# Performance work log

Measured on AMD Instinct MI355X. Metric: run time of the kernel, lower is better.

## Reference

```python
import jax, jax.numpy as jnp
import numpy as np

N = 4096      # nodes
D = 256       # input_dim
OUT = 256     # output_dim
K = 4         # num_kernels
TOPK = 16
CHEB_T = 2
ROW_TEMP = 1.0
EPS = 1e-9


def setup_inputs() -> dict:
    key = jax.random.key(0)
    ks = jax.random.split(key, 6)
    X = jax.random.normal(ks[0], (N, D), dtype=jnp.float32)
    L_k = jax.random.normal(ks[1], (K, D, D), dtype=jnp.float32) * 0.02
    alpha = jnp.ones((K,), dtype=jnp.float32)
    theta = jax.random.normal(ks[2], (CHEB_T + 1, D), dtype=jnp.float32) * 0.02
    rho_raw = jnp.zeros((), dtype=jnp.float32)
    proj_w = jax.random.normal(ks[3], (OUT, D), dtype=jnp.float32) / np.float32(np.sqrt(D))
    proj_b = jnp.zeros((OUT,), dtype=jnp.float32)
    v0 = jax.random.normal(ks[4], (N, 1), dtype=jnp.float32)  # power-iteration init
    return dict(X=X, L_k=L_k, alpha=alpha, theta=theta, rho_raw=rho_raw,
                proj_w=proj_w, proj_b=proj_b, v0=v0)


def reference(X, L_k, alpha, theta, rho_raw, proj_w, proj_b, v0):
    n, d = X.shape
    k = L_k.shape[0]
    # 1) kernel stack: A_k = X L_k X^T / sqrt(D), row softmax  -> (K,N,N)
    A = jnp.einsum('nd,kde,me->knm', X, L_k, X) / jnp.sqrt(jnp.float32(d))
    H_stack = jax.nn.softmax(A / max(ROW_TEMP, 1e-6), axis=-1)
    w = jax.nn.softmax(alpha)[:, None, None]
    H_fused = (H_stack * w).sum(0)                               # (N,N)
    # 2) soft incidence via per-row top-k + renormalize, scattered into B (N, K*N)
    vals, idx = jax.lax.top_k(H_stack, TOPK)                     # (K,N,TOPK)
    vals = vals / (vals.sum(-1, keepdims=True) + EPS)
    E = k * n
    cols = jnp.arange(k)[:, None, None] * n + jnp.arange(n)[None, :, None]
    cols = jnp.broadcast_to(cols, idx.shape)
    B = jnp.zeros((n, E), X.dtype).at[idx.reshape(-1), cols.reshape(-1)].set(vals.reshape(-1))
    W = jnp.ones((E,), X.dtype)
    # 3) hypergraph Laplacian L = I - Dv^{-1/2} B W De^{-1} B^T Dv^{-1/2}
    De = B.sum(0) + EPS
    Dv = (B * W[None, :]).sum(1) + EPS
    Dv_is = 1.0 / jnp.sqrt(Dv)
    S = (B * (W / De)[None, :]) @ B.T                            # (N,N)
    S_norm = Dv_is[:, None] * S * Dv_is[None, :]
    L = jnp.eye(n, dtype=X.dtype) - S_norm
    # 4) lambda_max via power iteration on detached L (constant, as in torch)
    Ld = jax.lax.stop_gradient(L)
    v = v0 / (jnp.linalg.norm(v0) + EPS)
    for _ in range(5):
        v = Ld @ v
        v = v / (jnp.linalg.norm(v) + EPS)
    lam = jnp.maximum((v.T @ (Ld @ v)).squeeze(), jnp.float32(1e-3))
    lam = jax.lax.stop_gradient(lam)
    # Chebyshev filter
    L_tilde = (2.0 / lam) * L - jnp.eye(n, dtype=X.dtype)
    out = X * theta[0][None, :]
    T0 = X
    T1 = L_tilde @ X
    out = out + T1 * theta[1][None, :]
    for t in range(2, CHEB_T + 1):
        T2 = 2.0 * (L_tilde @ T1) - T0
        out = out + T2 * theta[t][None, :]
        T0, T1 = T1, T2
    Z_spec = jax.nn.elu(out)
    # 5) residual blend with kernel diffusion
    Z_kern = H_fused @ X
    rho = jax.nn.sigmoid(rho_raw)
    Z_mix = rho * Z_spec + (1.0 - rho) * Z_kern
    # 6) final projection
    return Z_mix @ proj_w.T + proj_b[None, :]
```

## Files before the change

kernel.cpp:

```cpp
#include <hip/hip_runtime.h>
#include <math.h>

#define N_ 4096
#define D_ 256
#define K_ 4
#define TK_ 16
#define E_ (K_ * N_)
#define NENT_ (E_ * TK_)

typedef unsigned short u16;
typedef unsigned int u32;
typedef __attribute__((ext_vector_type(8))) short bf16x8;
typedef __attribute__((ext_vector_type(4))) float f32x4;

__device__ __forceinline__ u16 bf16_rne(float x) {
  u32 u = __float_as_uint(x);
  u32 r = u + 0x7FFFu + ((u >> 16) & 1u);
  return (u16)(r >> 16);
}


__global__ void scalars_kernel(const float* __restrict__ alpha,
                               const float* __restrict__ rho_raw,
                               float* __restrict__ scal) {
  if (threadIdx.x == 0) {
    float m = alpha[0];
    for (int k = 1; k < K_; ++k) m = fmaxf(m, alpha[k]);
    float e[K_]; float s = 0.f;
    for (int k = 0; k < K_; ++k) { e[k] = expf(alpha[k] - m); s += e[k]; }
    for (int k = 0; k < K_; ++k) scal[k] = e[k] / s;
    scal[4] = 1.0f / (1.0f + expf(-rho_raw[0]));
  }
}

__global__ void dvis_kernel(const float* __restrict__ DvAcc, float* __restrict__ Dvis) {
  int i = blockIdx.x * 256 + threadIdx.x;
  Dvis[i] = 1.0f / sqrtf(DvAcc[i] + 1e-9f);
}

__global__ void make_tkvd(const float* __restrict__ tkv, const int* __restrict__ tki,
                          const float* __restrict__ Dvis, float* __restrict__ tkvd) {
  int i = blockIdx.x * 256 + threadIdx.x;
  tkvd[i] = tkv[i] * Dvis[tki[i]];
}

__global__ void cvt_split4(const float* __restrict__ in, u16* __restrict__ hi,
                           u16* __restrict__ lo) {
  int i = (blockIdx.x * 256 + threadIdx.x) * 4;
  float4 v = *(const float4*)(in + i);
  u16 h0 = bf16_rne(v.x), h1 = bf16_rne(v.y), h2 = bf16_rne(v.z), h3 = bf16_rne(v.w);
  float f0 = __uint_as_float((u32)h0 << 16), f1 = __uint_as_float((u32)h1 << 16);
  float f2 = __uint_as_float((u32)h2 << 16), f3 = __uint_as_float((u32)h3 << 16);
  u16 l0 = bf16_rne(v.x - f0), l1 = bf16_rne(v.y - f1);
  u16 l2 = bf16_rne(v.z - f2), l3 = bf16_rne(v.w - f3);
  *(uint2*)(hi + i) = make_uint2((u32)h0 | ((u32)h1 << 16), (u32)h2 | ((u32)h3 << 16));
  *(uint2*)(lo + i) = make_uint2((u32)l0 | ((u32)l1 << 16), (u32)l2 | ((u32)l3 << 16));
}

__global__ __launch_bounds__(256) void transpose_split(const float* __restrict__ X,
                                                       u16* __restrict__ ht,
                                                       u16* __restrict__ lt) {
  __shared__ float tile[32][33];
  const int tx = threadIdx.x & 31, ty = threadIdx.x >> 5;
  const int d0 = blockIdx.x * 32, n0 = blockIdx.y * 32;
#pragma unroll
  for (int q = 0; q < 4; ++q)
    tile[ty + q * 8][tx] = X[(size_t)(n0 + ty + q * 8) * D_ + d0 + tx];
  __syncthreads();
#pragma unroll
  for (int q = 0; q < 4; ++q) {
    int dd = ty + q * 8;
    float v = tile[tx][dd];
    u16 h = bf16_rne(v);
    float hf = __uint_as_float((u32)h << 16);
    u16 l = bf16_rne(v - hf);
    ht[(size_t)(d0 + dd) * N_ + n0 + tx] = h;
    lt[(size_t)(d0 + dd) * N_ + n0 + tx] = l;
  }
}

__global__ __launch_bounds__(256) void gemm_nn64_split(const float* __restrict__ A,
                                                       const float* __restrict__ B,
                                                       u16* __restrict__ Ch,
                                                       u16* __restrict__ Cl,
                                                       int Kdim, int lda, int ldb, int ldc) {
  __shared__ float As[16][68];
  __shared__ float Bs[16][68];
  const int tid = threadIdx.x;
  const int bm = blockIdx.x * 64, bn = blockIdx.y * 64;
  const int lrA = tid >> 2, lcA = (tid & 3) * 4;
  const int rrB = tid >> 4, ccB = (tid & 15) * 4;
  const int tx = tid & 15, ty = tid >> 4;
  const float* Ap = A + (size_t)(bm + lrA) * lda + lcA;
  const float* Bp = B + (size_t)rrB * ldb + bn + ccB;
  float acc[4][4] = {};
  for (int k0 = 0; k0 < Kdim; k0 += 16) {
    float4 av = *(const float4*)(Ap + k0);
    float4 bv = *(const float4*)(Bp + (size_t)k0 * ldb);
    __syncthreads();
    As[lcA + 0][lrA] = av.x; As[lcA + 1][lrA] = av.y;
    As[lcA + 2][lrA] = av.z; As[lcA + 3][lrA] = av.w;
    *(float4*)&Bs[rrB][ccB] = bv;
    __syncthreads();
#pragma unroll
    for (int kk = 0; kk < 16; ++kk) {
      float a[4], b[4];
      *(float4*)a = *(const float4*)&As[kk][ty * 4];
      *(float4*)b = *(const float4*)&Bs[kk][tx * 4];
#pragma unroll
      for (int i = 0; i < 4; ++i)
#pragma unroll
        for (int j = 0; j < 4; ++j) acc[i][j] += a[i] * b[j];
    }
  }
#pragma unroll
  for (int i = 0; i < 4; ++i) {
    int row = bm + ty * 4 + i;
    u16 h[4], lo[4];
#pragma unroll
    for (int j = 0; j < 4; ++j) {
      h[j] = bf16_rne(acc[i][j]);
      lo[j] = bf16_rne(acc[i][j] - __uint_as_float((u32)h[j] << 16));
    }
    size_t base = (size_t)row * ldc + bn + tx * 4;
    *(uint2*)(Ch + base) = make_uint2((u32)h[0] | ((u32)h[1] << 16), (u32)h[2] | ((u32)h[3] << 16));
    *(uint2*)(Cl + base) = make_uint2((u32)lo[0] | ((u32)lo[1] << 16), (u32)lo[2] | ((u32)lo[3] << 16));
  }
}

__global__ __launch_bounds__(256) void gemm_nt64_bias(const float* __restrict__ A,
                                                      const float* __restrict__ B,
                                                      const float* __restrict__ bias,
                                                      float* __restrict__ C,
                                                      int Kdim, int lda, int ldb, int ldc) {
  __shared__ float As[16][68];
  __shared__ float Bs[16][68];
  const int tid = threadIdx.x;
  const int bm = blockIdx.x * 64, bn = blockIdx.y * 64;
  const int lr = tid >> 2, lc = (tid & 3) * 4;
  const int tx = tid & 15, ty = tid >> 4;
  const float* Ap = A + (size_t)(bm + lr) * lda + lc;
  const float* Bp = B + (size_t)(bn + lr) * ldb + lc;
  float acc[4][4] = {};
  for (int k0 = 0; k0 < Kdim; k0 += 16) {
    float4 av = *(const float4*)(Ap + k0);
    float4 bv = *(const float4*)(Bp + k0);
    __syncthreads();
    As[lc + 0][lr] = av.x; As[lc + 1][lr] = av.y; As[lc + 2][lr] = av.z; As[lc + 3][lr] = av.w;
    Bs[lc + 0][lr] = bv.x; Bs[lc + 1][lr] = bv.y; Bs[lc + 2][lr] = bv.z; Bs[lc + 3][lr] = bv.w;
    __syncthreads();
#pragma unroll
    for (int kk = 0; kk < 16; ++kk) {
      float a[4], b[4];
      *(float4*)a = *(const float4*)&As[kk][ty * 4];
      *(float4*)b = *(const float4*)&Bs[kk][tx * 4];
#pragma unroll
      for (int i = 0; i < 4; ++i)
#pragma unroll
        for (int j = 0; j < 4; ++j) acc[i][j] += a[i] * b[j];
    }
  }
#pragma unroll
  for (int i = 0; i < 4; ++i) {
    int row = bm + ty * 4 + i;
    float4 o;
    o.x = acc[i][0] + bias[bn + tx * 4 + 0];
    o.y = acc[i][1] + bias[bn + tx * 4 + 1];
    o.z = acc[i][2] + bias[bn + tx * 4 + 2];
    o.w = acc[i][3] + bias[bn + tx * 4 + 3];
    *(float4*)(C + (size_t)row * ldc + bn + tx * 4) = o;
  }
}


__global__ __launch_bounds__(256) void scores_mfma(const u16* __restrict__ Ahg,
                                                   const u16* __restrict__ Alg,
                                                   const u16* __restrict__ Bhg,
                                                   const u16* __restrict__ Blg,
                                                   float* __restrict__ C, float scale) {
  __shared__ char smem[65536];
  const int tid = threadIdx.x;
  const int bm = blockIdx.x * 128, bn = blockIdx.y * 128;
  const int w = tid >> 6, l = tid & 63;
  const int wr = (w >> 1) * 64, wc = (w & 1) * 64;
  const int srow = tid >> 3, scol = (tid & 7) * 8;
  const int lb = l & 15, lke = (l >> 4) * 8;
  const u16* bh0 = Bhg + (size_t)(bn + wc + 0  + lb) * D_ + lke;
  const u16* bh1 = Bhg + (size_t)(bn + wc + 16 + lb) * D_ + lke;
  const u16* bh2 = Bhg + (size_t)(bn + wc + 32 + lb) * D_ + lke;
  const u16* bh3 = Bhg + (size_t)(bn + wc + 48 + lb) * D_ + lke;
  const size_t dlo = (size_t)(Blg - Bhg);
  const int aoff[4] = {
    (srow + 0)  * 128 + ((scol * 2) ^ (((srow + 0)  & 7) << 4)),
    (srow + 32) * 128 + ((scol * 2) ^ (((srow + 32) & 7) << 4)),
    (srow + 64) * 128 + ((scol * 2) ^ (((srow + 64) & 7) << 4)),
    (srow + 96) * 128 + ((scol * 2) ^ (((srow + 96) & 7) << 4)) };
  f32x4 acc[4][4];
#pragma unroll
  for (int i = 0; i < 4; ++i)
#pragma unroll
    for (int j = 0; j < 4; ++j) { acc[i][j][0] = 0.f; acc[i][j][1] = 0.f; acc[i][j][2] = 0.f; acc[i][j][3] = 0.f; }

  uint4 ah[4], al[4];
#pragma unroll
  for (int ii = 0; ii < 4; ++ii) {
    int r = srow + ii * 32;
    ah[ii] = *(const uint4*)(Ahg + (size_t)(bm + r) * D_ + scol);
    al[ii] = *(const uint4*)(Alg + (size_t)(bm + r) * D_ + scol);
  }
  {
    char* bAh = smem; char* bAl = smem + 16384;
#pragma unroll
    for (int ii = 0; ii < 4; ++ii) {
      *(uint4*)(bAh + aoff[ii]) = ah[ii];
      *(uint4*)(bAl + aoff[ii]) = al[ii];
    }
  }
  __syncthreads();

  for (int c = 0; c < 4; ++c) {
    char* bAh = smem + ((c & 1) << 15);
    char* bAl = bAh + 16384;
    const bool hn = (c < 3);
    if (hn) {
      const int kn = (c + 1) * 64;
#pragma unroll
      for (int ii = 0; ii < 4; ++ii) {
        int r = srow + ii * 32;
        ah[ii] = *(const uint4*)(Ahg + (size_t)(bm + r) * D_ + kn + scol);
        al[ii] = *(const uint4*)(Alg + (size_t)(bm + r) * D_ + kn + scol);
      }
    }
#pragma unroll
    for (int kk = 0; kk < 2; ++kk) {
      const int kb = kk * 64 + ((l >> 4) << 4);
      const int ge = c * 64 + kk * 32;
      bf16x8 fbh[4], fbl[4];
      fbh[0] = *(const bf16x8*)(bh0 + ge); fbl[0] = *(const bf16x8*)(bh0 + dlo + ge);
      fbh[1] = *(const bf16x8*)(bh1 + ge); fbl[1] = *(const bf16x8*)(bh1 + dlo + ge);
      fbh[2] = *(const bf16x8*)(bh2 + ge); fbl[2] = *(const bf16x8*)(bh2 + dlo + ge);
      fbh[3] = *(const bf16x8*)(bh3 + ge); fbl[3] = *(const bf16x8*)(bh3 + dlo + ge);
#pragma unroll
      for (int i = 0; i < 4; ++i) {
        int ra = wr + i * 16 + lb;
        int oa = ra * 128 + (kb ^ ((ra & 7) << 4));
        bf16x8 fah = *(const bf16x8*)(bAh + oa);
        bf16x8 fal = *(const bf16x8*)(bAl + oa);
#pragma unroll
        for (int j = 0; j < 4; ++j) {
          acc[i][j] = __builtin_amdgcn_mfma_f32_16x16x32_bf16(fah, fbh[j], acc[i][j], 0, 0, 0);
          acc[i][j] = __builtin_amdgcn_mfma_f32_16x16x32_bf16(fah, fbl[j], acc[i][j], 0, 0, 0);
          acc[i][j] = __builtin_amdgcn_mfma_f32_16x16x32_bf16(fal, fbh[j], acc[i][j], 0, 0, 0);
        }
      }
    }
    if (hn) {
      char* nAh = smem + (((c + 1) & 1) << 15);
      char* nAl = nAh + 16384;
#pragma unroll
      for (int ii = 0; ii < 4; ++ii) {
        *(uint4*)(nAh + aoff[ii]) = ah[ii];
        *(uint4*)(nAl + aoff[ii]) = al[ii];
      }
    }
    __syncthreads();
  }
  float* Cs = (float*)smem;
  const int cr = (l >> 4) * 4, cc = l & 15;
#pragma unroll
  for (int p = 0; p < 2; ++p) {
    __syncthreads();
    if ((w >> 1) == p) {
#pragma unroll
      for (int i = 0; i < 4; ++i)
#pragma unroll
        for (int r = 0; r < 4; ++r) {
          int rl = i * 16 + cr + r;
          int sw = ((rl >> 2) & 3) << 4;
#pragma unroll
          for (int j = 0; j < 4; ++j) {
            int cl = wc + j * 16 + cc;
            Cs[rl * 128 + (cl ^ sw)] = acc[i][j][r] * scale;
          }
        }
    }
    __syncthreads();
#pragma unroll
    for (int ii = 0; ii < 8; ++ii) {
      int rl = ii * 8 + (tid >> 5);
      int c4 = (tid & 31) * 4;
      float4 v = *(float4*)&Cs[rl * 128 + (c4 ^ (((rl >> 2) & 3) << 4))];
      *(float4*)(C + (size_t)(bm + p * 64 + rl) * N_ + bn + c4) = v;
    }
  }
}

__global__ __launch_bounds__(256) void zkern_mfma(const u16* __restrict__ Hb,
                                                  const float* __restrict__ rowZ,
                                                  const u16* __restrict__ BhT,
                                                  const u16* __restrict__ BlT,
                                                  float* __restrict__ Zpart,
                                                  const float* __restrict__ scal,
                                                  int kidx, int kchunk, int accum) {
  __shared__ char smem[32768];
  const int tid = threadIdx.x;
  const int bm = blockIdx.x * 128, bn = blockIdx.y * 128;
  const int kz = blockIdx.z;
  const int w = tid >> 6, l = tid & 63;
  const int wr = (w >> 1) * 64, wc = (w & 1) * 64;
  const int hrow = tid >> 4, hcol = (tid & 15) * 4;
  const int lb = l & 15, lke = (l >> 4) * 8;
  const u16* bh0 = BhT + (size_t)(bn + wc + 0  + lb) * N_ + lke;
  const u16* bh1 = BhT + (size_t)(bn + wc + 16 + lb) * N_ + lke;
  const u16* bh2 = BhT + (size_t)(bn + wc + 32 + lb) * N_ + lke;
  const u16* bh3 = BhT + (size_t)(bn + wc + 48 + lb) * N_ + lke;
  const size_t dlo = (size_t)(BlT - BhT);
  int aoff[8];
#pragma unroll
  for (int ii = 0; ii < 8; ++ii) {
    int r = hrow + ii * 16;
    aoff[ii] = r * 128 + ((hcol * 2) ^ ((r & 7) << 4));
  }
  f32x4 acc[4][4];
#pragma unroll
  for (int i = 0; i < 4; ++i)
#pragma unroll
    for (int j = 0; j < 4; ++j) { acc[i][j][0] = 0.f; acc[i][j][1] = 0.f; acc[i][j][2] = 0.f; acc[i][j][3] = 0.f; }

  const int nchunk = kchunk >> 6;
  const int kbase = kz * kchunk;

  uint2 hv[8];
#pragma unroll
  for (int ii = 0; ii < 8; ++ii)
    hv[ii] = *(const uint2*)(Hb + (size_t)(bm + hrow + ii * 16) * N_ + kbase + hcol);
  {
    char* bAh = smem;
#pragma unroll
    for (int ii = 0; ii < 8; ++ii) *(uint2*)(bAh + aoff[ii]) = hv[ii];
  }
  __syncthreads();

  for (int c = 0; c < nchunk; ++c) {
    char* bAh = smem + ((c & 1) << 14);
    const bool hn = (c + 1 < nchunk);
    if (hn) {
      const int kn = kbase + (c + 1) * 64;
#pragma unroll
      for (int ii = 0; ii < 8; ++ii)
        hv[ii] = *(const uint2*)(Hb + (size_t)(bm + hrow + ii * 16) * N_ + kn + hcol);
    }
#pragma unroll
    for (int kk = 0; kk < 2; ++kk) {
      const int kb = kk * 64 + ((l >> 4) << 4);
      const int ge = kbase + c * 64 + kk * 32;
      bf16x8 fbh[4], fbl[4];
      fbh[0] = *(const bf16x8*)(bh0 + ge); fbl[0] = *(const bf16x8*)(bh0 + dlo + ge);
      fbh[1] = *(const bf16x8*)(bh1 + ge); fbl[1] = *(const bf16x8*)(bh1 + dlo + ge);
      fbh[2] = *(const bf16x8*)(bh2 + ge); fbl[2] = *(const bf16x8*)(bh2 + dlo + ge);
      fbh[3] = *(const bf16x8*)(bh3 + ge); fbl[3] = *(const bf16x8*)(bh3 + dlo + ge);
#pragma unroll
      for (int i = 0; i < 4; ++i) {
        int ra = wr + i * 16 + lb;
        int oa = ra * 128 + (kb ^ ((ra & 7) << 4));
        bf16x8 fah = *(const bf16x8*)(bAh + oa);
#pragma unroll
        for (int j = 0; j < 4; ++j) {
          acc[i][j] = __builtin_amdgcn_mfma_f32_16x16x32_bf16(fah, fbh[j], acc[i][j], 0, 0, 0);
          acc[i][j] = __builtin_amdgcn_mfma_f32_16x16x32_bf16(fah, fbl[j], acc[i][j], 0, 0, 0);
        }
      }
    }
    if (hn) {
      char* nAh = smem + (((c + 1) & 1) << 14);
#pragma unroll
      for (int ii = 0; ii < 8; ++ii) *(uint2*)(nAh + aoff[ii]) = hv[ii];
    }
    __syncthreads();
  }
  const float wk = scal[kidx];
  float* Zp = Zpart + (size_t)kz * N_ * D_;
  float* Cs = (float*)smem;
  const int cr = (l >> 4) * 4, cc = l & 15;
#pragma unroll
  for (int p = 0; p < 2; ++p) {
    __syncthreads();
    if ((w >> 1) == p) {
#pragma unroll
      for (int i = 0; i < 4; ++i)
#pragma unroll
        for (int r = 0; r < 4; ++r) {
          int rl = i * 16 + cr + r;
          int sw = ((rl >> 2) & 3) << 4;
#pragma unroll
          for (int j = 0; j < 4; ++j) {
            int cl = wc + j * 16 + cc;
            Cs[rl * 128 + (cl ^ sw)] = acc[i][j][r];
          }
        }
    }
    __syncthreads();
#pragma unroll
    for (int ii = 0; ii < 8; ++ii) {
      int rl = ii * 8 + (tid >> 5);
      int c4 = (tid & 31) * 4;
      int row = bm + p * 64 + rl;
      float sc = wk / rowZ[row];
      float4 v = *(float4*)&Cs[rl * 128 + (c4 ^ (((rl >> 2) & 3) << 4))];
      float* zb = Zp + (size_t)row * D_ + bn + c4;
      if (accum) {
        float4 z = *(float4*)zb;
        z.x += sc * v.x; z.y += sc * v.y; z.z += sc * v.z; z.w += sc * v.w;
        *(float4*)zb = z;
      } else {
        float4 z;
        z.x = sc * v.x; z.y = sc * v.y; z.z = sc * v.z; z.w = sc * v.w;
        *(float4*)zb = z;
      }
    }
  }
}

__global__ __launch_bounds__(256) void rowstats_topk(const float* __restrict__ S,
                                                     float* __restrict__ rowmax,
                                                     float* __restrict__ rowZ,
                                                     u16* __restrict__ Hb,
                                                     float* __restrict__ tkv,
                                                     int* __restrict__ tki) {
  const int row = blockIdx.x, tid = threadIdx.x;
  const int wid = tid >> 6, lane = tid & 63;
  __shared__ int hist[1024];
  __shared__ int P[256];
  __shared__ float cval[256];
  __shared__ int cgi[256];
  __shared__ int ccnt;
  __shared__ int binlo_s;
  __shared__ float rv[4];
  __shared__ float stk[TK_];
  __shared__ int itk[TK_];
  __shared__ float tv16[TK_];
  __shared__ float mzs[3];

  hist[tid] = 0; hist[tid + 256] = 0; hist[tid + 512] = 0; hist[tid + 768] = 0;
  if (tid == 0) ccnt = 0;

  const float4* Sp = (const float4*)(S + (size_t)row * N_);
  float r[16];
  float lmax = -3.4e38f;
#pragma unroll
  for (int it = 0; it < 4; ++it) {
    float4 v = Sp[tid + it * 256];
    r[it * 4 + 0] = v.x; r[it * 4 + 1] = v.y; r[it * 4 + 2] = v.z; r[it * 4 + 3] = v.w;
    lmax = fmaxf(lmax, fmaxf(fmaxf(v.x, v.y), fmaxf(v.z, v.w)));
  }
#pragma unroll
  for (int off = 32; off; off >>= 1) lmax = fmaxf(lmax, __shfl_xor(lmax, off));
  if (lane == 0) rv[wid] = lmax;
  __syncthreads();
  if (tid == 0) mzs[0] = fmaxf(fmaxf(rv[0], rv[1]), fmaxf(rv[2], rv[3]));
  __syncthreads();
  const float M = mzs[0];
  float eh[16];
  float ls = 0.f;
#pragma unroll
  for (int j = 0; j < 16; ++j) { eh[j] = expf(r[j] - M); ls += eh[j]; }
#pragma unroll
  for (int off = 32; off; off >>= 1) ls += __shfl_xor(ls, off);
  if (lane == 0) rv[wid] = ls;
  __syncthreads();
  if (tid == 0) {
    float z = rv[0] + rv[1] + rv[2] + rv[3];
    mzs[1] = z; rowmax[row] = M; rowZ[row] = z;
  }
  u16* Hrow = Hb + (size_t)row * N_;
#pragma unroll
  for (int it = 0; it < 4; ++it) {
    u16 h0 = bf16_rne(eh[it * 4 + 0]), h1 = bf16_rne(eh[it * 4 + 1]);
    u16 h2 = bf16_rne(eh[it * 4 + 2]), h3 = bf16_rne(eh[it * 4 + 3]);
    *(uint2*)(Hrow + it * 1024 + tid * 4) =
        make_uint2((u32)h0 | ((u32)h1 << 16), (u32)h2 | ((u32)h3 << 16));
  }
  __syncthreads();
  const float Z = mzs[1];

#pragma unroll
  for (int j = 0; j < 16; ++j) {
    u32 u = __float_as_uint(r[j]);
    u32 key = (u >> 31) ? ~u : (u | 0x80000000u);
    atomicAdd(&hist[key >> 22], 1);
  }
  __syncthreads();
  const int b0 = tid * 4;
  const int h0 = hist[b0], h1 = hist[b0 + 1], h2 = hist[b0 + 2], h3 = hist[b0 + 3];
  P[tid] = h0 + h1 + h2 + h3;
  __syncthreads();
  for (int o = 1; o < 256; o <<= 1) {
    int v = P[tid] + ((tid + o < 256) ? P[tid + o] : 0);
    __syncthreads();
    P[tid] = v;
    __syncthreads();
  }
  {
    int above = (tid < 255) ? P[tid + 1] : 0;
    int s3 = above + h3, s2 = s3 + h2, s1 = s2 + h1, s0 = s1 + h0;
    if (s3 >= TK_ && above < TK_) binlo_s = b0 + 3;
    else if (s2 >= TK_ && s3 < TK_) binlo_s = b0 + 2;
    else if (s1 >= TK_ && s2 < TK_) binlo_s = b0 + 1;
    else if (s0 >= TK_ && s1 < TK_) binlo_s = b0;
  }
  __syncthreads();
  const u32 kmin = (u32)binlo_s << 22;
#pragma unroll
  for (int j = 0; j < 16; ++j) {
    u32 u = __float_as_uint(r[j]);
    u32 key = (u >> 31) ? ~u : (u | 0x80000000u);
    if (key >= kmin) {
      int p = atomicAdd(&ccnt, 1);
      if (p < 256) {
        cval[p] = r[j];
        cgi[p] = 4 * tid + ((j >> 2) << 10) + (j & 3);
      }
    }
  }
  __syncthreads();
  const int nc = min(ccnt, 256);
  for (int t = 0; t < TK_; ++t) {
    if (tid < 64) {
      float bv = -3.4e38f; int bg = 0x7fffffff, bp = -1;
      for (int p = tid; p < nc; p += 64) {
        float v = cval[p]; int g = cgi[p];
        if (v > bv || (v == bv && g < bg)) { bv = v; bg = g; bp = p; }
      }
#pragma unroll
      for (int off = 32; off; off >>= 1) {
        float ov = __shfl_xor(bv, off);
        int og = __shfl_xor(bg, off);
        int op = __shfl_xor(bp, off);
        if (ov > bv || (ov == bv && og < bg)) { bv = ov; bg = og; bp = op; }
      }
      if (tid == 0) { stk[t] = bv; itk[t] = bg; cval[bp] = -3.4e38f; }
    }
    __syncthreads();
  }
  if (tid < TK_) tv16[tid] = expf(stk[tid] - M) / Z;
  __syncthreads();
  if (tid == 0) { float s = 0.f; for (int q = 0; q < TK_; ++q) s += tv16[q]; mzs[2] = s + 1e-9f; }
  __syncthreads();
  if (tid < TK_) {
    tkv[(size_t)row * TK_ + tid] = tv16[tid] / mzs[2];
    tki[(size_t)row * TK_ + tid] = itk[tid];
  }
}

__global__ void edge_scan(const float* __restrict__ tkv, const int* __restrict__ tki,
                          float* __restrict__ DvAcc, int* __restrict__ cnt,
                          float* __restrict__ invDe) {
  int e = blockIdx.x * 256 + threadIdx.x;
  float s = 0.f;
#pragma unroll
  for (int q = 0; q < TK_; ++q) s += tkv[(size_t)e * TK_ + q];
  invDe[e] = 1.0f / (s + 1e-9f);
#pragma unroll
  for (int q = 0; q < TK_; ++q) {
    int m = tki[(size_t)e * TK_ + q];
    atomicAdd(&DvAcc[m], tkv[(size_t)e * TK_ + q]);
    atomicAdd(&cnt[m], 1);
  }
}

__global__ __launch_bounds__(1024) void scan_offsets(const int* __restrict__ cnt,
                                                     int* __restrict__ off,
                                                     int* __restrict__ cur) {
  __shared__ int part[1024];
  const int t = threadIdx.x;
  const int b = t * 4;
  int c0 = cnt[b], c1 = cnt[b + 1], c2 = cnt[b + 2], c3 = cnt[b + 3];
  part[t] = c0 + c1 + c2 + c3;
  __syncthreads();
  for (int o = 1; o < 1024; o <<= 1) {
    int v = part[t] + ((t >= o) ? part[t - o] : 0);
    __syncthreads();
    part[t] = v;
    __syncthreads();
  }
  int ex = (t == 0) ? 0 : part[t - 1];
  off[b] = ex; off[b + 1] = ex + c0; off[b + 2] = ex + c0 + c1; off[b + 3] = ex + c0 + c1 + c2;
  cur[b] = off[b]; cur[b + 1] = off[b + 1]; cur[b + 2] = off[b + 2]; cur[b + 3] = off[b + 3];
  if (t == 1023) off[N_] = part[1023];
}

__global__ void edge_fill(const float* __restrict__ tkv, const int* __restrict__ tki,
                          int* __restrict__ cur, int* __restrict__ ince,
                          float* __restrict__ incv) {
  int e = blockIdx.x * 256 + threadIdx.x;
#pragma unroll
  for (int q = 0; q < TK_; ++q) {
    int m = tki[(size_t)e * TK_ + q];
    int pos = atomicAdd(&cur[m], 1);
    ince[pos] = e;
    incv[pos] = tkv[(size_t)e * TK_ + q];
  }
}

__global__ void pi_ye(const float* __restrict__ v, const float* __restrict__ tkvd,
                      const int* __restrict__ tki, const float* __restrict__ invDe,
                      float* __restrict__ ye) {
  int e = blockIdx.x * 256 + threadIdx.x;
  const float* tv = tkvd + (size_t)e * TK_;
  const int* ti = tki + (size_t)e * TK_;
  float a = 0.f;
#pragma unroll
  for (int q = 0; q < TK_; ++q) a += tv[q] * v[ti[q]];
  ye[e] = a * invDe[e];
}

__global__ void pi_step(const float* __restrict__ v, const float* __restrict__ ye,
                        const int* __restrict__ off, const int* __restrict__ ince,
                        const float* __restrict__ incv, const float* __restrict__ Dvis,
                        float* __restrict__ vn) {
  int m = blockIdx.x * 256 + threadIdx.x;
  float z = 0.f;
  int j0 = off[m], j1 = off[m + 1];
  for (int j = j0; j < j1; ++j) z += incv[j] * ye[ince[j]];
  vn[m] = v[m] - Dvis[m] * z;
}

__global__ __launch_bounds__(256) void pi_final(const float* __restrict__ v,
                                                const float* __restrict__ ye,
                                                const int* __restrict__ off,
                                                const int* __restrict__ ince,
                                                const float* __restrict__ incv,
                                                const float* __restrict__ Dvis,
                                                float* __restrict__ partial) {
  __shared__ float r1[256], r2[256];
  int m = blockIdx.x * 256 + threadIdx.x;
  float z = 0.f;
  int j0 = off[m], j1 = off[m + 1];
  for (int j = j0; j < j1; ++j) z += incv[j] * ye[ince[j]];
  float wv = v[m] - Dvis[m] * z;
  r1[threadIdx.x] = v[m] * wv;
  r2[threadIdx.x] = v[m] * v[m];
  __syncthreads();
  for (int s = 128; s; s >>= 1) {
    if (threadIdx.x < s) { r1[threadIdx.x] += r1[threadIdx.x + s]; r2[threadIdx.x] += r2[threadIdx.x + s]; }
    __syncthreads();
  }
  if (threadIdx.x == 0) { partial[blockIdx.x * 2] = r1[0]; partial[blockIdx.x * 2 + 1] = r2[0]; }
}

__global__ void pi_lam(const float* __restrict__ partial, float* __restrict__ scal) {
  if (threadIdx.x == 0) {
    float s1 = 0.f, s2 = 0.f;
    for (int b = 0; b < N_ / 256; ++b) { s1 += partial[2 * b]; s2 += partial[2 * b + 1]; }
    scal[5] = fmaxf(s1 / s2, 1e-3f);
  }
}

__global__ __launch_bounds__(256) void ye_mat(const float* __restrict__ M,
                                              const float* __restrict__ tkvd,
                                              const int* __restrict__ tki,
                                              const float* __restrict__ invDe,
                                              float* __restrict__ Ye) {
  const int w = threadIdx.x >> 6, l = threadIdx.x & 63;
  const int e = blockIdx.x * 4 + w;
  const float* tv = tkvd + (size_t)e * TK_;
  const int* ti = tki + (size_t)e * TK_;
  float4 a = make_float4(0.f, 0.f, 0.f, 0.f);
#pragma unroll
  for (int q = 0; q < TK_; ++q) {
    float v = tv[q];
    const float4 x = *(const float4*)(M + (size_t)ti[q] * D_ + l * 4);
    a.x += v * x.x; a.y += v * x.y; a.z += v * x.z; a.w += v * x.w;
  }
  const float s = invDe[e];
  float4 o; o.x = a.x * s; o.y = a.y * s; o.z = a.z * s; o.w = a.w * s;
  *(float4*)(Ye + (size_t)e * D_ + l * 4) = o;
}

__global__ __launch_bounds__(256) void bgather_combine(const float* __restrict__ Ye,
                                                       const int* __restrict__ off,
                                                       const int* __restrict__ ince,
                                                       const float* __restrict__ incv,
                                                       const float* __restrict__ Dvis,
                                                       const float* __restrict__ Mx,
                                                       const float* __restrict__ G,
                                                       const float* __restrict__ scal,
                                                       float* __restrict__ out, int mode) {
  const int w = threadIdx.x >> 6, l = threadIdx.x & 63;
  const int m = blockIdx.x * 4 + w;
  const int j0 = off[m], j1 = off[m + 1];
  float4 z = make_float4(0.f, 0.f, 0.f, 0.f);
  int j = j0;
  for (; j + 2 <= j1; j += 2) {
    float v0 = incv[j];     int e0 = ince[j];
    float v1 = incv[j + 1]; int e1 = ince[j + 1];
    float4 y0 = *(const float4*)(Ye + (size_t)e0 * D_ + l * 4);
    float4 y1 = *(const float4*)(Ye + (size_t)e1 * D_ + l * 4);
    z.x += v0 * y0.x + v1 * y1.x;
    z.y += v0 * y0.y + v1 * y1.y;
    z.z += v0 * y0.z + v1 * y1.z;
    z.w += v0 * y0.w + v1 * y1.w;
  }
  if (j < j1) {
    float v0 = incv[j]; int e0 = ince[j];
    float4 y0 = *(const float4*)(Ye + (size_t)e0 * D_ + l * 4);
    z.x += v0 * y0.x; z.y += v0 * y0.y; z.z += v0 * y0.z; z.w += v0 * y0.w;
  }
  const float lam = scal[5];
  const float c = 2.0f / lam;
  const float dv = Dvis[m];
  const size_t idx = (size_t)m * D_ + l * 4;
  float4 mx = *(const float4*)(Mx + idx);
  float4 o;
  if (mode == 1) {
    o.x = (c - 1.0f) * mx.x - c * dv * z.x;
    o.y = (c - 1.0f) * mx.y - c * dv * z.y;
    o.z = (c - 1.0f) * mx.z - c * dv * z.z;
    o.w = (c - 1.0f) * mx.w - c * dv * z.w;
  } else {
    float4 g = *(const float4*)(G + idx);
    o.x = (2.0f * c - 2.0f) * mx.x - 2.0f * c * dv * z.x - g.x;
    o.y = (2.0f * c - 2.0f) * mx.y - 2.0f * c * dv * z.y - g.y;
    o.z = (2.0f * c - 2.0f) * mx.z - 2.0f * c * dv * z.z - g.z;
    o.w = (2.0f * c - 2.0f) * mx.w - 2.0f * c * dv * z.w - g.w;
  }
  *(float4*)(out + idx) = o;
}

__global__ void mix_kernel(const float* __restrict__ X, const float* __restrict__ T1,
                           const float* __restrict__ T2, const float* __restrict__ theta,
                           const float* __restrict__ Zpart, int splitk,
                           const float* __restrict__ scal, float* __restrict__ Zmix) {
  const int i = blockIdx.x * 256 + threadIdx.x;
  const int d = i & (D_ - 1);
  float cheb = X[i] * theta[d] + T1[i] * theta[D_ + d] + T2[i] * theta[2 * D_ + d];
  float zs = cheb > 0.f ? cheb : expm1f(cheb);
  float zk = 0.f;
  for (int s = 0; s < splitk; ++s) zk += Zpart[(size_t)s * N_ * D_ + i];
  const float rho = scal[4];
  Zmix[i] = rho * zs + (1.0f - rho) * zk;
}


extern "C" void kernel_launch(void* const* d_in, const int* in_sizes, int n_in,
                              void* d_out, int out_size, void* d_ws, size_t ws_size,
                              hipStream_t stream) {
  const float* X       = (const float*)d_in[0];
  const float* L_k     = (const float*)d_in[1];
  const float* alpha   = (const float*)d_in[2];
  const float* theta   = (const float*)d_in[3];
  const float* rho_raw = (const float*)d_in[4];
  const float* proj_w  = (const float*)d_in[5];
  const float* proj_b  = (const float*)d_in[6];
  const float* v0      = (const float*)d_in[7];
  float* out = (float*)d_out;

  char* w = (char*)d_ws;
  size_t o = 0;
  auto alloc = [&](size_t bytes) -> char* {
    char* p = w + o; o += (bytes + 255) & ~(size_t)255; return p;
  };
  float* S     = (float*)alloc((size_t)N_ * N_ * 4);
  u16*   Hb    = (u16*)  alloc((size_t)N_ * N_ * 2);
  u16*   Xh    = (u16*)  alloc((size_t)N_ * D_ * 2);
  u16*   Xl    = (u16*)  alloc((size_t)N_ * D_ * 2);
  u16*   XhT   = (u16*)  alloc((size_t)D_ * N_ * 2);
  u16*   XlT   = (u16*)  alloc((size_t)D_ * N_ * 2);
  u16*   XLh   = (u16*)  alloc((size_t)N_ * D_ * 2);
  u16*   XLl   = (u16*)  alloc((size_t)N_ * D_ * 2);
  float* rowmax= (float*)alloc(N_ * 4);
  float* rowZ  = (float*)alloc(N_ * 4);
  float* tkv   = (float*)alloc((size_t)NENT_ * 4);
  int*   tki   = (int*)  alloc((size_t)NENT_ * 4);
  float* tkvd  = (float*)alloc((size_t)NENT_ * 4);
  float* invDe = (float*)alloc(E_ * 4);
  float* DvAcc = (float*)alloc(N_ * 4);
  float* Dvis  = (float*)alloc(N_ * 4);
  int*   cnt   = (int*)  alloc(N_ * 4);
  int*   off   = (int*)  alloc((N_ + 1) * 4);
  int*   cur   = (int*)  alloc(N_ * 4);
  int*   ince  = (int*)  alloc((size_t)NENT_ * 4);
  float* incv  = (float*)alloc((size_t)NENT_ * 4);
  float* va    = (float*)alloc(N_ * 4);
  float* vbuf  = (float*)alloc(N_ * 4);
  float* yev   = (float*)alloc(E_ * 4);
  float* part  = (float*)alloc((N_ / 256) * 2 * 4);
  float* scal  = (float*)alloc(256);
  int SPLITK = 8;
  while (SPLITK > 1 && o + (size_t)SPLITK * N_ * D_ * 4 > ws_size) SPLITK >>= 1;
  float* Zpart = (float*)alloc((size_t)SPLITK * N_ * D_ * 4);
  const int kchunk = N_ / SPLITK;
  float* Ye   = S + (size_t)N_ * D_;
  float* T1   = Ye + (size_t)E_ * D_;
  float* T2   = T1 + (size_t)N_ * D_;
  float* Zmix = T2 + (size_t)N_ * D_;

  scalars_kernel<<<1, 64, 0, stream>>>(alpha, rho_raw, scal);
  hipMemsetAsync(DvAcc, 0, N_ * 4, stream);
  hipMemsetAsync(cnt, 0, N_ * 4, stream);

  cvt_split4<<<(N_ * D_ / 4) / 256, 256, 0, stream>>>(X, Xh, Xl);
  transpose_split<<<dim3(D_ / 32, N_ / 32), 256, 0, stream>>>(X, XhT, XlT);

  for (int k = 0; k < K_; ++k) {
    gemm_nn64_split<<<dim3(N_ / 64, D_ / 64), 256, 0, stream>>>(
        X, L_k + (size_t)k * D_ * D_, XLh, XLl, D_, D_, D_, D_);
    scores_mfma<<<dim3(N_ / 128, N_ / 128), 256, 0, stream>>>(
        XLh, XLl, Xh, Xl, S, 1.0f / 16.0f);
    rowstats_topk<<<N_, 256, 0, stream>>>(
        S, rowmax, rowZ, Hb, tkv + (size_t)k * N_ * TK_, tki + (size_t)k * N_ * TK_);
    zkern_mfma<<<dim3(N_ / 128, D_ / 128, SPLITK), 256, 0, stream>>>(
        Hb, rowZ, XhT, XlT, Zpart, scal, k, kchunk, (k > 0) ? 1 : 0);
  }

  edge_scan<<<E_ / 256, 256, 0, stream>>>(tkv, tki, DvAcc, cnt, invDe);
  dvis_kernel<<<N_ / 256, 256, 0, stream>>>(DvAcc, Dvis);
  make_tkvd<<<NENT_ / 256, 256, 0, stream>>>(tkv, tki, Dvis, tkvd);
  scan_offsets<<<1, 1024, 0, stream>>>(cnt, off, cur);
  edge_fill<<<E_ / 256, 256, 0, stream>>>(tkv, tki, cur, ince, incv);

  const float* vc = v0;
  float* vn = va;
  for (int it = 0; it < 5; ++it) {
    pi_ye<<<E_ / 256, 256, 0, stream>>>(vc, tkvd, tki, invDe, yev);
    pi_step<<<N_ / 256, 256, 0, stream>>>(vc, yev, off, ince, incv, Dvis, vn);
    vc = vn;
    vn = (vc == va) ? vbuf : va;
  }
  pi_ye<<<E_ / 256, 256, 0, stream>>>(vc, tkvd, tki, invDe, yev);
  pi_final<<<N_ / 256, 256, 0, stream>>>(vc, yev, off, ince, incv, Dvis, part);
  pi_lam<<<1, 64, 0, stream>>>(part, scal);

  ye_mat<<<E_ / 4, 256, 0, stream>>>(X, tkvd, tki, invDe, Ye);
  bgather_combine<<<N_ / 4, 256, 0, stream>>>(Ye, off, ince, incv, Dvis, X, X, scal, T1, 1);
  ye_mat<<<E_ / 4, 256, 0, stream>>>(T1, tkvd, tki, invDe, Ye);
  bgather_combine<<<N_ / 4, 256, 0, stream>>>(Ye, off, ince, incv, Dvis, T1, X, scal, T2, 2);

  mix_kernel<<<N_ * D_ / 256, 256, 0, stream>>>(X, T1, T2, theta, Zpart, SPLITK, scal, Zmix);

  gemm_nt64_bias<<<dim3(N_ / 64, D_ / 64), 256, 0, stream>>>(
      Zmix, proj_w, proj_b, out, D_, D_, D_, D_);
}
```

Measured before the change: 1.191 ms.

## Use MFMA for X·L_k and fuse power iteration into one cooperative kernel

Replaces the fp32 SIMT GEMM computing X·L_k with a bf16 split-precision MFMA kernel. L_k is pre-transposed and split once into high and low bf16 parts. Separately, the twelve small power-iteration launches are merged into one cooperative kernel that uses grid-wide syncs between steps, cutting launch overhead. The cooperative launch needs all 64 blocks to be co-resident, and the three-term bf16 split adds a small precision change.

```diff
diff --git a/kernel.cpp b/kernel.cpp
--- a/kernel.cpp
+++ b/kernel.cpp
@@ -1,4 +1,5 @@
 #include <hip/hip_runtime.h>
+#include <hip/hip_cooperative_groups.h>
 #include <math.h>
 
 #define N_ 4096
@@ -79,52 +80,28 @@
   }
 }
 
-__global__ __launch_bounds__(256) void gemm_nn64_split(const float* __restrict__ A,
-                                                       const float* __restrict__ B,
-                                                       u16* __restrict__ Ch,
-                                                       u16* __restrict__ Cl,
-                                                       int Kdim, int lda, int ldb, int ldc) {
-  __shared__ float As[16][68];
-  __shared__ float Bs[16][68];
-  const int tid = threadIdx.x;
-  const int bm = blockIdx.x * 64, bn = blockIdx.y * 64;
-  const int lrA = tid >> 2, lcA = (tid & 3) * 4;
-  const int rrB = tid >> 4, ccB = (tid & 15) * 4;
-  const int tx = tid & 15, ty = tid >> 4;
-  const float* Ap = A + (size_t)(bm + lrA) * lda + lcA;
-  const float* Bp = B + (size_t)rrB * ldb + bn + ccB;
-  float acc[4][4] = {};
-  for (int k0 = 0; k0 < Kdim; k0 += 16) {
-    float4 av = *(const float4*)(Ap + k0);
-    float4 bv = *(const float4*)(Bp + (size_t)k0 * ldb);
-    __syncthreads();
-    As[lcA + 0][lrA] = av.x; As[lcA + 1][lrA] = av.y;
-    As[lcA + 2][lrA] = av.z; As[lcA + 3][lrA] = av.w;
-    *(float4*)&Bs[rrB][ccB] = bv;
-    __syncthreads();
-#pragma unroll
-    for (int kk = 0; kk < 16; ++kk) {
-      float a[4], b[4];
-      *(float4*)a = *(const float4*)&As[kk][ty * 4];
-      *(float4*)b = *(const float4*)&Bs[kk][tx * 4];
-#pragma unroll
-      for (int i = 0; i < 4; ++i)
-#pragma unroll
-        for (int j = 0; j < 4; ++j) acc[i][j] += a[i] * b[j];
-    }
-  }
-#pragma unroll
-  for (int i = 0; i < 4; ++i) {
-    int row = bm + ty * 4 + i;
-    u16 h[4], lo[4];
-#pragma unroll
-    for (int j = 0; j < 4; ++j) {
-      h[j] = bf16_rne(acc[i][j]);
-      lo[j] = bf16_rne(acc[i][j] - __uint_as_float((u32)h[j] << 16));
-    }
-    size_t base = (size_t)row * ldc + bn + tx * 4;
-    *(uint2*)(Ch + base) = make_uint2((u32)h[0] | ((u32)h[1] << 16), (u32)h[2] | ((u32)h[3] << 16));
-    *(uint2*)(Cl + base) = make_uint2((u32)lo[0] | ((u32)lo[1] << 16), (u32)lo[2] | ((u32)lo[3] << 16));
+__global__ __launch_bounds__(256) void transpose_split_L(const float* __restrict__ L,
+                                                         u16* __restrict__ lth,
+                                                         u16* __restrict__ ltl) {
+  __shared__ float tile[32][33];
+  const int tx = threadIdx.x & 31, ty = threadIdx.x >> 5;
+  const int n0 = blockIdx.x * 32, k0 = blockIdx.y * 32, kk = blockIdx.z;
+  const float* Lk = L + (size_t)kk * D_ * D_;
+#pragma unroll
+  for (int q = 0; q < 4; ++q)
+    tile[ty + q * 8][tx] = Lk[(size_t)(k0 + ty + q * 8) * D_ + n0 + tx];
+  __syncthreads();
+  u16* ho = lth + (size_t)kk * D_ * D_;
+  u16* lo = ltl + (size_t)kk * D_ * D_;
+#pragma unroll
+  for (int q = 0; q < 4; ++q) {
+    int nn = ty + q * 8;
+    float v = tile[tx][nn];
+    u16 h = bf16_rne(v);
+    float hf = __uint_as_float((u32)h << 16);
+    u16 l = bf16_rne(v - hf);
+    ho[(size_t)(n0 + nn) * D_ + k0 + tx] = h;
+    lo[(size_t)(n0 + nn) * D_ + k0 + tx] = l;
   }
 }
 
@@ -172,6 +149,138 @@
   }
 }
 
+
+__global__ __launch_bounds__(256) void xl_mfma(const u16* __restrict__ Ahg,
+                                               const u16* __restrict__ Alg,
+                                               const u16* __restrict__ Bhg,
+                                               const u16* __restrict__ Blg,
+                                               u16* __restrict__ Ch,
+                                               u16* __restrict__ Cl) {
+  __shared__ char smem[65536];
+  const int tid = threadIdx.x;
+  const int bm = blockIdx.x * 128, bn = blockIdx.y * 128;
+  const int w = tid >> 6, l = tid & 63;
+  const int wr = (w >> 1) * 64, wc = (w & 1) * 64;
+  const int srow = tid >> 3, scol = (tid & 7) * 8;
+  const int lb = l & 15, lke = (l >> 4) * 8;
+  const u16* bh0 = Bhg + (size_t)(bn + wc + 0  + lb) * D_ + lke;
+  const u16* bh1 = Bhg + (size_t)(bn + wc + 16 + lb) * D_ + lke;
+  const u16* bh2 = Bhg + (size_t)(bn + wc + 32 + lb) * D_ + lke;
+  const u16* bh3 = Bhg + (size_t)(bn + wc + 48 + lb) * D_ + lke;
+  const size_t dlo = (size_t)(Blg - Bhg);
+  const int aoff[4] = {
+    (srow + 0)  * 128 + ((scol * 2) ^ (((srow + 0)  & 7) << 4)),
+    (srow + 32) * 128 + ((scol * 2) ^ (((srow + 32) & 7) << 4)),
+    (srow + 64) * 128 + ((scol * 2) ^ (((srow + 64) & 7) << 4)),
+    (srow + 96) * 128 + ((scol * 2) ^ (((srow + 96) & 7) << 4)) };
+  f32x4 acc[4][4];
+#pragma unroll
+  for (int i = 0; i < 4; ++i)
+#pragma unroll
+    for (int j = 0; j < 4; ++j) { acc[i][j][0] = 0.f; acc[i][j][1] = 0.f; acc[i][j][2] = 0.f; acc[i][j][3] = 0.f; }
+
+  uint4 ah[4], al[4];
+#pragma unroll
+  for (int ii = 0; ii < 4; ++ii) {
+    int r = srow + ii * 32;
+    ah[ii] = *(const uint4*)(Ahg + (size_t)(bm + r) * D_ + scol);
+    al[ii] = *(const uint4*)(Alg + (size_t)(bm + r) * D_ + scol);
+  }
+  {
+    char* bAh = smem; char* bAl = smem + 16384;
+#pragma unroll
+    for (int ii = 0; ii < 4; ++ii) {
+      *(uint4*)(bAh + aoff[ii]) = ah[ii];
+      *(uint4*)(bAl + aoff[ii]) = al[ii];
+    }
+  }
+  __syncthreads();
+
+  for (int c = 0; c < 4; ++c) {
+    char* bAh = smem + ((c & 1) << 15);
+    char* bAl = bAh + 16384;
+    const bool hn = (c < 3);
+    if (hn) {
+      const int kn = (c + 1) * 64;
+#pragma unroll
+      for (int ii = 0; ii < 4; ++ii) {
+        int r = srow + ii * 32;
+        ah[ii] = *(const uint4*)(Ahg + (size_t)(bm + r) * D_ + kn + scol);
+        al[ii] = *(const uint4*)(Alg + (size_t)(bm + r) * D_ + kn + scol);
+      }
+    }
+#pragma unroll
+    for (int kk = 0; kk < 2; ++kk) {
+      const int kb = kk * 64 + ((l >> 4) << 4);
+      const int ge = c * 64 + kk * 32;
+      bf16x8 fbh[4], fbl[4];
+      fbh[0] = *(const bf16x8*)(bh0 + ge); fbl[0] = *(const bf16x8*)(bh0 + dlo + ge);
+      fbh[1] = *(const bf16x8*)(bh1 + ge); fbl[1] = *(const bf16x8*)(bh1 + dlo + ge);
+      fbh[2] = *(const bf16x8*)(bh2 + ge); fbl[2] = *(const bf16x8*)(bh2 + dlo + ge);
+      fbh[3] = *(const bf16x8*)(bh3 + ge); fbl[3] = *(const bf16x8*)(bh3 + dlo + ge);
+#pragma unroll
+      for (int i = 0; i < 4; ++i) {
+        int ra = wr + i * 16 + lb;
+        int oa = ra * 128 + (kb ^ ((ra & 7) << 4));
+        bf16x8 fah = *(const bf16x8*)(bAh + oa);
+        bf16x8 fal = *(const bf16x8*)(bAl + oa);
+#pragma unroll
+        for (int j = 0; j < 4; ++j) {
+          acc[i][j] = __builtin_amdgcn_mfma_f32_16x16x32_bf16(fah, fbh[j], acc[i][j], 0, 0, 0);
+          acc[i][j] = __builtin_amdgcn_mfma_f32_16x16x32_bf16(fah, fbl[j], acc[i][j], 0, 0, 0);
+          acc[i][j] = __builtin_amdgcn_mfma_f32_16x16x32_bf16(fal, fbh[j], acc[i][j], 0, 0, 0);
+        }
+      }
+    }
+    if (hn) {
+      char* nAh = smem + (((c + 1) & 1) << 15);
+      char* nAl = nAh + 16384;
+#pragma unroll
+      for (int ii = 0; ii < 4; ++ii) {
+        *(uint4*)(nAh + aoff[ii]) = ah[ii];
+        *(uint4*)(nAl + aoff[ii]) = al[ii];
+      }
+    }
+    __syncthreads();
+  }
+  float* Cs = (float*)smem;
+  const int cr = (l >> 4) * 4, cc = l & 15;
+#pragma unroll
+  for (int p = 0; p < 2; ++p) {
+    __syncthreads();
+    if ((w >> 1) == p) {
+#pragma unroll
+      for (int i = 0; i < 4; ++i)
+#pragma unroll
+        for (int r = 0; r < 4; ++r) {
+          int rl = i * 16 + cr + r;
+          int sw = ((rl >> 2) & 3) << 4;
+#pragma unroll
+          for (int j = 0; j < 4; ++j) {
+            int cl = wc + j * 16 + cc;
+            Cs[rl * 128 + (cl ^ sw)] = acc[i][j][r];
+          }
+        }
+    }
+    __syncthreads();
+#pragma unroll
+    for (int ii = 0; ii < 8; ++ii) {
+      int rl = ii * 8 + (tid >> 5);
+      int c4 = (tid & 31) * 4;
+      float4 v = *(float4*)&Cs[rl * 128 + (c4 ^ (((rl >> 2) & 3) << 4))];
+      int row = bm + p * 64 + rl;
+      u16 h0 = bf16_rne(v.x), h1 = bf16_rne(v.y), h2 = bf16_rne(v.z), h3 = bf16_rne(v.w);
+      u16 l0 = bf16_rne(v.x - __uint_as_float((u32)h0 << 16));
+      u16 l1 = bf16_rne(v.y - __uint_as_float((u32)h1 << 16));
+      u16 l2 = bf16_rne(v.z - __uint_as_float((u32)h2 << 16));
+      u16 l3 = bf16_rne(v.w - __uint_as_float((u32)h3 << 16));
+      *(uint2*)(Ch + (size_t)row * D_ + bn + c4) =
+          make_uint2((u32)h0 | ((u32)h1 << 16), (u32)h2 | ((u32)h3 << 16));
+      *(uint2*)(Cl + (size_t)row * D_ + bn + c4) =
+          make_uint2((u32)l0 | ((u32)l1 << 16), (u32)l2 | ((u32)l3 << 16));
+    }
+  }
+}
 
 __global__ __launch_bounds__(256) void scores_mfma(const u16* __restrict__ Ahg,
                                                    const u16* __restrict__ Alg,
@@ -602,54 +711,65 @@
   }
 }
 
-__global__ void pi_ye(const float* __restrict__ v, const float* __restrict__ tkvd,
-                      const int* __restrict__ tki, const float* __restrict__ invDe,
-                      float* __restrict__ ye) {
-  int e = blockIdx.x * 256 + threadIdx.x;
-  const float* tv = tkvd + (size_t)e * TK_;
-  const int* ti = tki + (size_t)e * TK_;
-  float a = 0.f;
-#pragma unroll
-  for (int q = 0; q < TK_; ++q) a += tv[q] * v[ti[q]];
-  ye[e] = a * invDe[e];
-}
-
-__global__ void pi_step(const float* __restrict__ v, const float* __restrict__ ye,
-                        const int* __restrict__ off, const int* __restrict__ ince,
-                        const float* __restrict__ incv, const float* __restrict__ Dvis,
-                        float* __restrict__ vn) {
-  int m = blockIdx.x * 256 + threadIdx.x;
-  float z = 0.f;
-  int j0 = off[m], j1 = off[m + 1];
-  for (int j = j0; j < j1; ++j) z += incv[j] * ye[ince[j]];
-  vn[m] = v[m] - Dvis[m] * z;
-}
-
-__global__ __launch_bounds__(256) void pi_final(const float* __restrict__ v,
-                                                const float* __restrict__ ye,
-                                                const int* __restrict__ off,
-                                                const int* __restrict__ ince,
-                                                const float* __restrict__ incv,
-                                                const float* __restrict__ Dvis,
-                                                float* __restrict__ partial) {
+__global__ void pi_fused(const float* __restrict__ v0, const float* __restrict__ tkvd,
+                         const int* __restrict__ tki, const float* __restrict__ invDe,
+                         const int* __restrict__ off, const int* __restrict__ ince,
+                         const float* __restrict__ incv, const float* __restrict__ Dvis,
+                         float* __restrict__ va, float* __restrict__ vb2,
+                         float* __restrict__ ye, float* __restrict__ partial,
+                         float* __restrict__ scal) {
+  namespace cg = cooperative_groups;
+  cg::grid_group g = cg::this_grid();
+  const int gid = blockIdx.x * 256 + threadIdx.x;
+  const float* vc = v0;
+  float* vn = va;
+  for (int it = 0; it < 5; ++it) {
+    {
+      const float* tv = tkvd + (size_t)gid * TK_;
+      const int* ti = tki + (size_t)gid * TK_;
+      float a = 0.f;
+#pragma unroll
+      for (int q = 0; q < TK_; ++q) a += tv[q] * vc[ti[q]];
+      ye[gid] = a * invDe[gid];
+    }
+    g.sync();
+    if (gid < N_) {
+      float z = 0.f;
+      int j0 = off[gid], j1 = off[gid + 1];
+      for (int j = j0; j < j1; ++j) z += incv[j] * ye[ince[j]];
+      vn[gid] = vc[gid] - Dvis[gid] * z;
+    }
+    g.sync();
+    vc = vn;
+    vn = (vc == va) ? vb2 : va;
+  }
+  {
+    const float* tv = tkvd + (size_t)gid * TK_;
+    const int* ti = tki + (size_t)gid * TK_;
+    float a = 0.f;
+#pragma unroll
+    for (int q = 0; q < TK_; ++q) a += tv[q] * vc[ti[q]];
+    ye[gid] = a * invDe[gid];
+  }
+  g.sync();
   __shared__ float r1[256], r2[256];
-  int m = blockIdx.x * 256 + threadIdx.x;
-  float z = 0.f;
-  int j0 = off[m], j1 = off[m + 1];
-  for (int j = j0; j < j1; ++j) z += incv[j] * ye[ince[j]];
-  float wv = v[m] - Dvis[m] * z;
-  r1[threadIdx.x] = v[m] * wv;
-  r2[threadIdx.x] = v[m] * v[m];
-  __syncthreads();
-  for (int s = 128; s; s >>= 1) {
-    if (threadIdx.x < s) { r1[threadIdx.x] += r1[threadIdx.x + s]; r2[threadIdx.x] += r2[threadIdx.x + s]; }
-    __syncthreads();
-  }
-  if (threadIdx.x == 0) { partial[blockIdx.x * 2] = r1[0]; partial[blockIdx.x * 2 + 1] = r2[0]; }
-}
-
-__global__ void pi_lam(const float* __restrict__ partial, float* __restrict__ scal) {
-  if (threadIdx.x == 0) {
+  if (blockIdx.x < N_ / 256) {
+    int m = gid;
+    float z = 0.f;
+    int j0 = off[m], j1 = off[m + 1];
+    for (int j = j0; j < j1; ++j) z += incv[j] * ye[ince[j]];
+    float wv = vc[m] - Dvis[m] * z;
+    r1[threadIdx.x] = vc[m] * wv;
+    r2[threadIdx.x] = vc[m] * vc[m];
+    __syncthreads();
+    for (int s = 128; s; s >>= 1) {
+      if (threadIdx.x < s) { r1[threadIdx.x] += r1[threadIdx.x + s]; r2[threadIdx.x] += r2[threadIdx.x + s]; }
+      __syncthreads();
+    }
+    if (threadIdx.x == 0) { partial[blockIdx.x * 2] = r1[0]; partial[blockIdx.x * 2 + 1] = r2[0]; }
+  }
+  g.sync();
+  if (gid == 0) {
     float s1 = 0.f, s2 = 0.f;
     for (int b = 0; b < N_ / 256; ++b) { s1 += partial[2 * b]; s2 += partial[2 * b + 1]; }
     scal[5] = fmaxf(s1 / s2, 1e-3f);
@@ -718,11 +838,11 @@
     o.z = (c - 1.0f) * mx.z - c * dv * z.z;
     o.w = (c - 1.0f) * mx.w - c * dv * z.w;
   } else {
-    float4 g = *(const float4*)(G + idx);
-    o.x = (2.0f * c - 2.0f) * mx.x - 2.0f * c * dv * z.x - g.x;
-    o.y = (2.0f * c - 2.0f) * mx.y - 2.0f * c * dv * z.y - g.y;
-    o.z = (2.0f * c - 2.0f) * mx.z - 2.0f * c * dv * z.z - g.z;
-    o.w = (2.0f * c - 2.0f) * mx.w - 2.0f * c * dv * z.w - g.w;
+    float4 gg = *(const float4*)(G + idx);
+    o.x = (2.0f * c - 2.0f) * mx.x - 2.0f * c * dv * z.x - gg.x;
+    o.y = (2.0f * c - 2.0f) * mx.y - 2.0f * c * dv * z.y - gg.y;
+    o.z = (2.0f * c - 2.0f) * mx.z - 2.0f * c * dv * z.z - gg.z;
+    o.w = (2.0f * c - 2.0f) * mx.w - 2.0f * c * dv * z.w - gg.w;
   }
   *(float4*)(out + idx) = o;
 }
@@ -768,6 +888,8 @@
   u16*   XlT   = (u16*)  alloc((size_t)D_ * N_ * 2);
   u16*   XLh   = (u16*)  alloc((size_t)N_ * D_ * 2);
   u16*   XLl   = (u16*)  alloc((size_t)N_ * D_ * 2);
+  u16*   LTh   = (u16*)  alloc((size_t)K_ * D_ * D_ * 2);
+  u16*   LTl   = (u16*)  alloc((size_t)K_ * D_ * D_ * 2);
   float* rowmax= (float*)alloc(N_ * 4);
   float* rowZ  = (float*)alloc(N_ * 4);
   float* tkv   = (float*)alloc((size_t)NENT_ * 4);
@@ -801,10 +923,11 @@
 
   cvt_split4<<<(N_ * D_ / 4) / 256, 256, 0, stream>>>(X, Xh, Xl);
   transpose_split<<<dim3(D_ / 32, N_ / 32), 256, 0, stream>>>(X, XhT, XlT);
+  transpose_split_L<<<dim3(D_ / 32, D_ / 32, K_), 256, 0, stream>>>(L_k, LTh, LTl);
 
   for (int k = 0; k < K_; ++k) {
-    gemm_nn64_split<<<dim3(N_ / 64, D_ / 64), 256, 0, stream>>>(
-        X, L_k + (size_t)k * D_ * D_, XLh, XLl, D_, D_, D_, D_);
+    xl_mfma<<<dim3(N_ / 128, D_ / 128), 256, 0, stream>>>(
+        Xh, Xl, LTh + (size_t)k * D_ * D_, LTl + (size_t)k * D_ * D_, XLh, XLl);
     scores_mfma<<<dim3(N_ / 128, N_ / 128), 256, 0, stream>>>(
         XLh, XLl, Xh, Xl, S, 1.0f / 16.0f);
     rowstats_topk<<<N_, 256, 0, stream>>>(
@@ -819,17 +942,14 @@
   scan_offsets<<<1, 1024, 0, stream>>>(cnt, off, cur);
   edge_fill<<<E_ / 256, 256, 0, stream>>>(tkv, tki, cur, ince, incv);
 
-  const float* vc = v0;
-  float* vn = va;
-  for (int it = 0; it < 5; ++it) {
-    pi_ye<<<E_ / 256, 256, 0, stream>>>(vc, tkvd, tki, invDe, yev);
-    pi_step<<<N_ / 256, 256, 0, stream>>>(vc, yev, off, ince, incv, Dvis, vn);
-    vc = vn;
-    vn = (vc == va) ? vbuf : va;
-  }
-  pi_ye<<<E_ / 256, 256, 0, stream>>>(vc, tkvd, tki, invDe, yev);
-  pi_final<<<N_ / 256, 256, 0, stream>>>(vc, yev, off, ince, incv, Dvis, part);
-  pi_lam<<<1, 64, 0, stream>>>(part, scal);
+  {
+    void* pf_args[] = {(void*)&v0, (void*)&tkvd, (void*)&tki, (void*)&invDe,
+                       (void*)&off, (void*)&ince, (void*)&incv, (void*)&Dvis,
+                       (void*)&va, (void*)&vbuf, (void*)&yev, (void*)&part,
+                       (void*)&scal};
+    hipLaunchCooperativeKernel((const void*)pi_fused, dim3(E_ / 256), dim3(256),
+                               pf_args, 0, stream);
+  }
 
   ye_mat<<<E_ / 4, 256, 0, stream>>>(X, tkvd, tki, invDe, Ye);
   bgather_combine<<<N_ / 4, 256, 0, stream>>>(Ye, off, ince, incv, Dvis, X, X, scal, T1, 1);
```

Measured after the change: 1.306 ms. 1.1x slower.
